# Kernel tuning notes

Hardware: AMD Instinct MI355X
Metric: run time of the kernel (lower is better)

## Reference

```python
import jax, jax.numpy as jnp
import numpy as np

N = 100000   # num nodes
E = 3200000  # num edges (avg degree 32)
EPS = 1e-5   # BatchNorm eps


def _gcn_norm(edge_index, edge_weight, n):
    # add self loops with weight 1 (PyG gcn_norm default fill_value=1.0)
    loops = jnp.arange(n, dtype=edge_index.dtype)
    ei = jnp.concatenate([edge_index, jnp.stack([loops, loops])], axis=1)
    ew = jnp.concatenate([edge_weight, jnp.ones((n,), edge_weight.dtype)])
    row, col = ei[0], ei[1]
    deg = jax.ops.segment_sum(ew, col, num_segments=n)
    deg_safe = jnp.where(deg > 0, deg, 1.0)
    dinv = jnp.where(deg > 0, jax.lax.rsqrt(deg_safe), 0.0)
    norm = dinv[row] * ew * dinv[col]  # [E+N]
    return row, col, norm


def _gcn_conv(x, row, col, norm, W, b, n):
    h = x @ W                                   # [N, out]
    msg = h[row] * norm[:, None]                # gather + scale, [E+N, out]
    out = jax.ops.segment_sum(msg, col, num_segments=n)  # scatter-add
    return out + b


def _bn(x, g, b, rm, rv):
    # BatchNorm1d in eval mode: running statistics
    return (x - rm) * jax.lax.rsqrt(rv + EPS) * g + b


def setup_inputs() -> dict:
    key = jax.random.key(0)
    ks = jax.random.split(key, 24)
    def p(i, shape, scale=1.0):
        return jax.random.normal(ks[i], shape, dtype=jnp.float32) * scale
    inp = {
        "x": p(0, (N, 1)),
        "edge_index": jax.random.randint(ks[1], (2, E), 0, N, dtype=jnp.int32),
        "edge_weight": jax.random.uniform(ks[2], (E,), dtype=jnp.float32),
        # GCNConv weights (glorot-ish scale) and biases
        "W1": p(3, (1, 16), 0.5), "b1": jnp.zeros((16,), jnp.float32),
        "W2": p(4, (16, 4), 0.25), "b2": jnp.zeros((4,), jnp.float32),
        "W3": p(5, (4, 1), 0.5), "b3": jnp.zeros((1,), jnp.float32),
        # BatchNorm params + running stats (running_var > 0)
        "g1": p(6, (16,), 0.1) + 1.0, "be1": p(7, (16,), 0.1),
        "rm1": p(8, (16,), 0.1), "rv1": jax.random.uniform(ks[9], (16,)) + 0.5,
        "g2": p(10, (4,), 0.1) + 1.0, "be2": p(11, (4,), 0.1),
        "rm2": p(12, (4,), 0.1), "rv2": jax.random.uniform(ks[13], (4,)) + 0.5,
        "g3": p(14, (1,), 0.1) + 1.0, "be3": p(15, (1,), 0.1),
        "rm3": p(16, (1,), 0.1), "rv3": jax.random.uniform(ks[17], (1,)) + 0.5,
        # end Linear(1, 1)
        "Wl": p(18, (1, 1)), "bl": p(19, (1,), 0.1),
    }
    return inp


def reference(x, edge_index, edge_weight,
              W1, b1, W2, b2, W3, b3,
              g1, be1, rm1, rv1,
              g2, be2, rm2, rv2,
              g3, be3, rm3, rv3,
              Wl, bl):
    row, col, norm = _gcn_norm(edge_index, edge_weight, N)
    h = _gcn_conv(x, row, col, norm, W1, b1, N)
    h = jax.nn.relu(_bn(h, g1, be1, rm1, rv1))  # dropout = identity in eval
    h = _gcn_conv(h, row, col, norm, W2, b2, N)
    h = jax.nn.relu(_bn(h, g2, be2, rm2, rv2))
    h = _gcn_conv(h, row, col, norm, W3, b3, N)
    h = _bn(h, g3, be3, rm3, rv3)
    h = h @ Wl + bl
    return jax.nn.sigmoid(h)
```

## Files before the change

kernel.cpp:

```cpp
#include <hip/hip_runtime.h>
#include <math.h>

#define NN 100000
#define NE 3200000
#define EPSBN 1e-5f

#define BSH 7
#define NB 782
#define NBLK 500
#define CHUNK 6400
#define C4 (CHUNK/4)
#define CAP 5120
#define BTA 512

#define STCAP 4608
#define NCOL 100096

__global__ void k_params_zero(const float* __restrict__ W1, const float* __restrict__ b1,
                              const float* __restrict__ g1, const float* __restrict__ be1,
                              const float* __restrict__ rm1, const float* __restrict__ rv1,
                              const float* __restrict__ b2,
                              const float* __restrict__ g2, const float* __restrict__ be2,
                              const float* __restrict__ rm2, const float* __restrict__ rv2,
                              const float* __restrict__ b3,
                              const float* __restrict__ g3, const float* __restrict__ be3,
                              const float* __restrict__ rm3, const float* __restrict__ rv3,
                              const float* __restrict__ Wl, const float* __restrict__ bl,
                              float* __restrict__ P, int* __restrict__ cnt) {
    int f = threadIdx.x;
    for (int i = f; i < NB; i += 1024) cnt[i] = 0;
    if (f < 16) {
        float k = g1[f] * rsqrtf(rv1[f] + EPSBN);
        P[f]      = W1[f] * k;
        P[16 + f] = (b1[f] - rm1[f]) * k + be1[f];
    }
    if (f < 4) {
        float k = g2[f] * rsqrtf(rv2[f] + EPSBN);
        P[32 + f] = k;
        P[36 + f] = (b2[f] - rm2[f]) * k + be2[f];
    }
    if (f == 0) {
        float k = g3[0] * rsqrtf(rv3[0] + EPSBN);
        P[40] = k * Wl[0];
        P[41] = ((b3[0] - rm3[0]) * k + be3[0]) * Wl[0] + bl[0];
    }
}

__global__ void k_build(const int* __restrict__ row, const int* __restrict__ col,
                        const float* __restrict__ ew, int* __restrict__ cnt,
                        uint2* __restrict__ rec) {
    __shared__ int h[NB];
    __shared__ int gb[NB];
    __shared__ int gsum[98];
    __shared__ uint2 st[CHUNK];
    __shared__ unsigned short sb[CHUNK];
    int blk = blockIdx.x, tid = threadIdx.x;
    for (int j = tid; j < NB; j += BTA) h[j] = 0;
    __syncthreads();

    const int4* c4 = (const int4*)(col + blk * CHUNK);
    int rk[4][4];
#pragma unroll
    for (int it = 0; it < 4; ++it) {
        int i = tid + it * BTA;
        if (i < C4) {
            int4 c = c4[i];
            rk[it][0] = atomicAdd(&h[c.x >> BSH], 1);
            rk[it][1] = atomicAdd(&h[c.y >> BSH], 1);
            rk[it][2] = atomicAdd(&h[c.z >> BSH], 1);
            rk[it][3] = atomicAdd(&h[c.w >> BSH], 1);
        }
    }
    __syncthreads();

    for (int j = tid; j < NB; j += BTA) {
        int hj = h[j];
        gb[j] = hj ? atomicAdd(&cnt[j], hj) : 0;
    }

    if (tid < 98) {
        int s = 0, b0 = tid * 8;
#pragma unroll
        for (int k = 0; k < 8; ++k) { int idx = b0 + k; s += (idx < NB) ? h[idx] : 0; }
        gsum[tid] = s;
    }
    __syncthreads();
    if (tid == 0) {
        int run = 0;
        for (int g = 0; g < 98; ++g) { int t = gsum[g]; gsum[g] = run; run += t; }
    }
    __syncthreads();
    if (tid < 98) {
        int run = gsum[tid], b0 = tid * 8;
#pragma unroll
        for (int k = 0; k < 8; ++k) {
            int idx = b0 + k;
            if (idx < NB) { int t = h[idx]; h[idx] = run; run += t; }
        }
    }
    __syncthreads();

    const int4*   r4 = (const int4*)(row + blk * CHUNK);
    const float4* w4 = (const float4*)(ew + blk * CHUNK);
#pragma unroll
    for (int it = 0; it < 4; ++it) {
        int i = tid + it * BTA;
        if (i < C4) {
            int4 c = c4[i]; int4 r = r4[i]; float4 w = w4[i];
            int b0 = c.x >> BSH, b1 = c.y >> BSH, b2 = c.z >> BSH, b3 = c.w >> BSH;
            int s0 = h[b0] + rk[it][0];
            st[s0] = make_uint2((unsigned)r.x | ((unsigned)(c.x & 127) << 17), __float_as_uint(w.x));
            sb[s0] = (unsigned short)b0;
            int s1 = h[b1] + rk[it][1];
            st[s1] = make_uint2((unsigned)r.y | ((unsigned)(c.y & 127) << 17), __float_as_uint(w.y));
            sb[s1] = (unsigned short)b1;
            int s2 = h[b2] + rk[it][2];
            st[s2] = make_uint2((unsigned)r.z | ((unsigned)(c.z & 127) << 17), __float_as_uint(w.z));
            sb[s2] = (unsigned short)b2;
            int s3 = h[b3] + rk[it][3];
            st[s3] = make_uint2((unsigned)r.w | ((unsigned)(c.w & 127) << 17), __float_as_uint(w.w));
            sb[s3] = (unsigned short)b3;
        }
    }
    __syncthreads();

    for (int i = tid; i < CHUNK; i += BTA) {
        int b = sb[i];
        rec[(size_t)b * CAP + gb[b] + (i - h[b])] = st[i];
    }
}

__global__ void k_subsort_deg(const int* __restrict__ cnt, uint2* __restrict__ rec,
                              int2* __restrict__ colsc, const float* __restrict__ x,
                              float* __restrict__ dinv, float* __restrict__ xd) {
    __shared__ uint2 st[STCAP];
    __shared__ int subtot[128];
    __shared__ int colbase[128];
    int bin = blockIdx.x, tid = threadIdx.x;
    int lane = tid & 63, wv = tid >> 6;
    int n = cnt[bin];
    if (n > STCAP) n = STCAP;
    uint2* rb = rec + (size_t)bin * CAP;

    uint2 r[9];
#pragma unroll
    for (int k = 0; k < 9; ++k) {
        int i = tid + k * BTA;
        if (i < n) r[k] = rb[i];
    }
    if (tid < 128) subtot[tid] = 0;
    __syncthreads();

    int rk[9];
#pragma unroll
    for (int k = 0; k < 9; ++k) {
        int i = tid + k * BTA;
        if (i < n) {
            unsigned key = (r[k].x >> 17) & 127u;
            rk[k] = atomicAdd(&subtot[key], 1);
        }
    }
    __syncthreads();

    if (wv == 0) {
        int a = subtot[2 * lane], b = subtot[2 * lane + 1];
        int s = a + b;
#pragma unroll
        for (int off = 1; off < 64; off <<= 1) {
            int t = __shfl_up(s, off);
            if (lane >= off) s += t;
        }
        int excl = s - (a + b);
        colbase[2 * lane] = excl;
        colbase[2 * lane + 1] = excl + a;
    }
    __syncthreads();

    if (tid < 128)
        colsc[bin * 128 + tid] = make_int2(bin * CAP + colbase[tid], subtot[tid]);

#pragma unroll
    for (int k = 0; k < 9; ++k) {
        int i = tid + k * BTA;
        if (i < n) {
            unsigned key = (r[k].x >> 17) & 127u;
            st[colbase[key] + rk[k]] = r[k];
        }
    }
    __syncthreads();

    for (int i = tid; i < n; i += BTA) rb[i] = st[i];

    for (int pass = 0; pass < 2; ++pass) {
        int cl = pass * 64 + (tid >> 3);
        int j = tid & 7;
        int cb = colbase[cl], cc = subtot[cl];
        float a = 0.f;
        for (int i = j; i < cc; i += 8) a += __uint_as_float(st[cb + i].y);
        a += __shfl_xor(a, 1); a += __shfl_xor(a, 2); a += __shfl_xor(a, 4);
        int colv = (bin << BSH) + cl;
        if (j == 0 && colv < NN) {
            float d = rsqrtf(1.0f + a);
            dinv[colv] = d;
            xd[colv] = x[colv] * d;
        }
    }
}


__global__ void k_agg1_8(const int2* __restrict__ colsc, const uint2* __restrict__ rec,
                         const float* __restrict__ dinv, const float* __restrict__ xd,
                         const float* __restrict__ P, const float* __restrict__ W2,
                         float* __restrict__ m2s) {
    int tid = threadIdx.x;
    int col = blockIdx.x * 64 + (tid >> 3);
    int j = tid & 7;
    if (col >= NN) return;
    int2 sc = colsc[col];
    const uint2* p = rec + sc.x;
    float a = 0.f;
    for (int i = j; i < sc.y; i += 8) {
        uint2 v = p[i];
        a += xd[v.x & 0x1FFFF] * __uint_as_float(v.y);
    }
    a += __shfl_xor(a, 1); a += __shfl_xor(a, 2); a += __shfl_xor(a, 4);
    if (j == 0) {
        float dc = dinv[col];
        float y = (a + xd[col]) * dc;
        float m0 = 0.f, m1 = 0.f, m2v = 0.f, m3v = 0.f;
#pragma unroll
        for (int f = 0; f < 16; ++f) {
            float z = fmaxf(fmaf(y, P[f], P[16 + f]), 0.0f);
            m0 = fmaf(z, W2[f * 4 + 0], m0);
            m1 = fmaf(z, W2[f * 4 + 1], m1);
            m2v = fmaf(z, W2[f * 4 + 2], m2v);
            m3v = fmaf(z, W2[f * 4 + 3], m3v);
        }
        *(float4*)(m2s + 4 * col) = make_float4(m0 * dc, m1 * dc, m2v * dc, m3v * dc);
    }
}

__global__ void k_agg2_8(const int2* __restrict__ colsc, const uint2* __restrict__ rec,
                         const float* __restrict__ dinv, const float* __restrict__ m2s,
                         const float* __restrict__ P, const float* __restrict__ W3,
                         float* __restrict__ m3s) {
    int tid = threadIdx.x;
    int col = blockIdx.x * 64 + (tid >> 3);
    int j = tid & 7;
    if (col >= NN) return;
    int2 sc = colsc[col];
    const uint2* p = rec + sc.x;
    float a0 = 0.f, a1 = 0.f, a2 = 0.f, a3 = 0.f;
    for (int i = j; i < sc.y; i += 8) {
        uint2 v = p[i];
        float w = __uint_as_float(v.y);
        float4 m = *(const float4*)(m2s + 4 * (v.x & 0x1FFFF));
        a0 = fmaf(m.x, w, a0);
        a1 = fmaf(m.y, w, a1);
        a2 = fmaf(m.z, w, a2);
        a3 = fmaf(m.w, w, a3);
    }
    a0 += __shfl_xor(a0, 1); a0 += __shfl_xor(a0, 2); a0 += __shfl_xor(a0, 4);
    a1 += __shfl_xor(a1, 1); a1 += __shfl_xor(a1, 2); a1 += __shfl_xor(a1, 4);
    a2 += __shfl_xor(a2, 1); a2 += __shfl_xor(a2, 2); a2 += __shfl_xor(a2, 4);
    a3 += __shfl_xor(a3, 1); a3 += __shfl_xor(a3, 2); a3 += __shfl_xor(a3, 4);
    if (j == 0) {
        float dc = dinv[col];
        float4 mc = *(const float4*)(m2s + 4 * col);
        float b0 = (a0 + mc.x) * dc;
        float b1 = (a1 + mc.y) * dc;
        float b2 = (a2 + mc.z) * dc;
        float b3 = (a3 + mc.w) * dc;
        float v3 = 0.f;
        v3 = fmaf(fmaxf(fmaf(b0, P[32], P[36]), 0.f), W3[0], v3);
        v3 = fmaf(fmaxf(fmaf(b1, P[33], P[37]), 0.f), W3[1], v3);
        v3 = fmaf(fmaxf(fmaf(b2, P[34], P[38]), 0.f), W3[2], v3);
        v3 = fmaf(fmaxf(fmaf(b3, P[35], P[39]), 0.f), W3[3], v3);
        m3s[col] = v3 * dc;
    }
}

__global__ void k_agg3_8(const int2* __restrict__ colsc, const uint2* __restrict__ rec,
                         const float* __restrict__ dinv, const float* __restrict__ m3s,
                         const float* __restrict__ P, float* __restrict__ out) {
    int tid = threadIdx.x;
    int col = blockIdx.x * 64 + (tid >> 3);
    int j = tid & 7;
    if (col >= NN) return;
    int2 sc = colsc[col];
    const uint2* p = rec + sc.x;
    float a = 0.f;
    for (int i = j; i < sc.y; i += 8) {
        uint2 v = p[i];
        a += m3s[v.x & 0x1FFFF] * __uint_as_float(v.y);
    }
    a += __shfl_xor(a, 1); a += __shfl_xor(a, 2); a += __shfl_xor(a, 4);
    if (j == 0) {
        float t = fmaf((a + m3s[col]) * dinv[col], P[40], P[41]);
        out[col] = 1.0f / (1.0f + __expf(-t));
    }
}


__global__ void k_init_deg(float* __restrict__ deg) {
    int i = blockIdx.x * blockDim.x + threadIdx.x;
    if (i < NN) deg[i] = 1.0f;
}

__global__ void k_dinv_y1(const float* __restrict__ deg, const float* __restrict__ x,
                          float* __restrict__ dinv, float* __restrict__ y1) {
    int i = blockIdx.x * blockDim.x + threadIdx.x;
    if (i >= NN) return;
    float d = rsqrtf(deg[i]);
    dinv[i] = d;
    y1[i] = x[i] * d * d;
}

__global__ void k_l1_epi(const float* __restrict__ y1, const float* __restrict__ dinv,
                         const float* __restrict__ P, const float* __restrict__ W2,
                         float* __restrict__ m2, float* __restrict__ agg2) {
    int i = blockIdx.x * blockDim.x + threadIdx.x;
    if (i >= NN) return;
    float y = y1[i];
    float m0 = 0.f, m1 = 0.f, m2v = 0.f, m3v = 0.f;
#pragma unroll
    for (int f = 0; f < 16; ++f) {
        float z = fmaxf(fmaf(y, P[f], P[16 + f]), 0.0f);
        m0 = fmaf(z, W2[f * 4 + 0], m0);
        m1 = fmaf(z, W2[f * 4 + 1], m1);
        m2v = fmaf(z, W2[f * 4 + 2], m2v);
        m3v = fmaf(z, W2[f * 4 + 3], m3v);
    }
    float d = dinv[i];
    float d2 = d * d;
    *(float4*)(m2 + 4 * i)   = make_float4(m0, m1, m2v, m3v);
    *(float4*)(agg2 + 4 * i) = make_float4(m0 * d2, m1 * d2, m2v * d2, m3v * d2);
}

__global__ void k_l2_epi(const float* __restrict__ agg2, const float* __restrict__ dinv,
                         const float* __restrict__ P, const float* __restrict__ W3,
                         float* __restrict__ m3, float* __restrict__ agg3) {
    int i = blockIdx.x * blockDim.x + threadIdx.x;
    if (i >= NN) return;
    float4 a = *(const float4*)(agg2 + 4 * i);
    float v = 0.f;
    v = fmaf(fmaxf(fmaf(a.x, P[32], P[36]), 0.f), W3[0], v);
    v = fmaf(fmaxf(fmaf(a.y, P[33], P[37]), 0.f), W3[1], v);
    v = fmaf(fmaxf(fmaf(a.z, P[34], P[38]), 0.f), W3[2], v);
    v = fmaf(fmaxf(fmaf(a.w, P[35], P[39]), 0.f), W3[3], v);
    float d = dinv[i];
    m3[i] = v;
    agg3[i] = v * d * d;
}

__global__ void k_final(const float* __restrict__ agg3, const float* __restrict__ P,
                        float* __restrict__ out) {
    int i = blockIdx.x * blockDim.x + threadIdx.x;
    if (i >= NN) return;
    float t = fmaf(agg3[i], P[40], P[41]);
    out[i] = 1.0f / (1.0f + __expf(-t));
}

__global__ void k_deg(const int* __restrict__ col, const float* __restrict__ ew,
                      float* __restrict__ deg) {
    int e = (blockIdx.x * blockDim.x + threadIdx.x) * 4;
    if (e >= NE) return;
    int4 c = *(const int4*)(col + e);
    float4 w = *(const float4*)(ew + e);
    atomicAdd(&deg[c.x], w.x);
    atomicAdd(&deg[c.y], w.y);
    atomicAdd(&deg[c.z], w.z);
    atomicAdd(&deg[c.w], w.w);
}

__global__ void k_norm_agg1(const int* __restrict__ row, const int* __restrict__ col,
                            const float* __restrict__ ew, const float* __restrict__ dinv,
                            const float* __restrict__ x,
                            float* __restrict__ norm, float* __restrict__ y1) {
    int e = (blockIdx.x * blockDim.x + threadIdx.x) * 4;
    if (e >= NE) return;
    int4 r = *(const int4*)(row + e);
    int4 c = *(const int4*)(col + e);
    float4 w = *(const float4*)(ew + e);
    float4 nv;
    nv.x = dinv[r.x] * w.x * dinv[c.x];
    nv.y = dinv[r.y] * w.y * dinv[c.y];
    nv.z = dinv[r.z] * w.z * dinv[c.z];
    nv.w = dinv[r.w] * w.w * dinv[c.w];
    *(float4*)(norm + e) = nv;
    atomicAdd(&y1[c.x], x[r.x] * nv.x);
    atomicAdd(&y1[c.y], x[r.y] * nv.y);
    atomicAdd(&y1[c.z], x[r.z] * nv.z);
    atomicAdd(&y1[c.w], x[r.w] * nv.w);
}

__global__ void k_agg2(const int* __restrict__ row, const int* __restrict__ col,
                       const float* __restrict__ norm, const float* __restrict__ m2,
                       float* __restrict__ agg2) {
    int e = blockIdx.x * blockDim.x + threadIdx.x;
    if (e >= NE) return;
    int r = row[e], c = col[e];
    float nv = norm[e];
    float4 m = *(const float4*)(m2 + 4 * r);
    atomicAdd(&agg2[4 * c + 0], m.x * nv);
    atomicAdd(&agg2[4 * c + 1], m.y * nv);
    atomicAdd(&agg2[4 * c + 2], m.z * nv);
    atomicAdd(&agg2[4 * c + 3], m.w * nv);
}

__global__ void k_agg3(const int* __restrict__ row, const int* __restrict__ col,
                       const float* __restrict__ norm, const float* __restrict__ m3,
                       float* __restrict__ agg3) {
    int e = (blockIdx.x * blockDim.x + threadIdx.x) * 4;
    if (e >= NE) return;
    int4 r = *(const int4*)(row + e);
    int4 c = *(const int4*)(col + e);
    float4 nv = *(const float4*)(norm + e);
    atomicAdd(&agg3[c.x], m3[r.x] * nv.x);
    atomicAdd(&agg3[c.y], m3[r.y] * nv.y);
    atomicAdd(&agg3[c.z], m3[r.z] * nv.z);
    atomicAdd(&agg3[c.w], m3[r.w] * nv.w);
}


extern "C" void kernel_launch(void* const* d_in, const int* in_sizes, int n_in,
                              void* d_out, int out_size, void* d_ws, size_t ws_size,
                              hipStream_t stream) {
    const float* x  = (const float*)d_in[0];
    const int*   ei = (const int*)d_in[1];
    const float* ew = (const float*)d_in[2];
    const float* W1 = (const float*)d_in[3];
    const float* b1 = (const float*)d_in[4];
    const float* W2 = (const float*)d_in[5];
    const float* b2 = (const float*)d_in[6];
    const float* W3 = (const float*)d_in[7];
    const float* b3 = (const float*)d_in[8];
    const float* g1 = (const float*)d_in[9];
    const float* be1 = (const float*)d_in[10];
    const float* rm1 = (const float*)d_in[11];
    const float* rv1 = (const float*)d_in[12];
    const float* g2 = (const float*)d_in[13];
    const float* be2 = (const float*)d_in[14];
    const float* rm2 = (const float*)d_in[15];
    const float* rv2 = (const float*)d_in[16];
    const float* g3 = (const float*)d_in[17];
    const float* be3 = (const float*)d_in[18];
    const float* rm3 = (const float*)d_in[19];
    const float* rv3 = (const float*)d_in[20];
    const float* Wl = (const float*)d_in[21];
    const float* bl = (const float*)d_in[22];
    float* out = (float*)d_out;

    const int* row = ei;
    const int* col = ei + NE;

    const int BT = 256;
    const int gN = (NN + BT - 1) / BT;
    const int gE4 = (NE / 4 + BT - 1) / BT;
    const int gC8 = NCOL / 64;

    char* ws = (char*)d_ws;

    if (ws_size >= 36800000u) {
        float* P     = (float*)(ws);
        int*   cnt   = (int*)  (ws + 4096);
        int2*  colsc = (int2*) (ws + 16384);
        float* dinv  = (float*)(ws + 1048576);
        float* xd    = (float*)(ws + 1572864);
        float* m3s   = (float*)(ws + 2097152);
        float* m2s   = (float*)(ws + 2621440);
        uint2* rec   = (uint2*)(ws + 4718592);

        k_params_zero<<<1, 1024, 0, stream>>>(W1, b1, g1, be1, rm1, rv1,
                                              b2, g2, be2, rm2, rv2,
                                              b3, g3, be3, rm3, rv3, Wl, bl, P, cnt);
        k_build<<<NBLK, BTA, 0, stream>>>(row, col, ew, cnt, rec);
        k_subsort_deg<<<NB, BTA, 0, stream>>>(cnt, rec, colsc, x, dinv, xd);
        k_agg1_8<<<gC8, BTA, 0, stream>>>(colsc, rec, dinv, xd, P, W2, m2s);
        k_agg2_8<<<gC8, BTA, 0, stream>>>(colsc, rec, dinv, m2s, P, W3, m3s);
        k_agg3_8<<<gC8, BTA, 0, stream>>>(colsc, rec, dinv, m3s, P, out);
    } else {
        float* deg   = (float*)(ws);
        float* dinv  = (float*)(ws + 400000);
        float* y1    = (float*)(ws + 800000);
        float* m2    = (float*)(ws + 1200000);
        float* agg2  = (float*)(ws + 2800000);
        float* m3    = (float*)(ws + 4400000);
        float* agg3  = (float*)(ws + 4800000);
        float* Pf    = (float*)(ws + 5200000);
        float* norm  = (float*)(ws + 5200256);
        const int gE1 = (NE + BT - 1) / BT;

        k_params_zero<<<1, 1024, 0, stream>>>(W1, b1, g1, be1, rm1, rv1,
                                              b2, g2, be2, rm2, rv2,
                                              b3, g3, be3, rm3, rv3, Wl, bl, Pf, (int*)(ws + 5300000));
        k_init_deg<<<gN, BT, 0, stream>>>(deg);
        k_deg<<<gE4, BT, 0, stream>>>(col, ew, deg);
        k_dinv_y1<<<gN, BT, 0, stream>>>(deg, x, dinv, y1);
        k_norm_agg1<<<gE4, BT, 0, stream>>>(row, col, ew, dinv, x, norm, y1);
        k_l1_epi<<<gN, BT, 0, stream>>>(y1, dinv, Pf, W2, m2, agg2);
        k_agg2<<<gE1, BT, 0, stream>>>(row, col, norm, m2, agg2);
        k_l2_epi<<<gN, BT, 0, stream>>>(agg2, dinv, Pf, W3, m3, agg3);
        k_agg3<<<gE4, BT, 0, stream>>>(row, col, norm, m3, agg3);
        k_final<<<gN, BT, 0, stream>>>(agg3, Pf, out);
    }
}
```

Baseline: 109.7 us.

## Vectorize record scatter/sort with 16-byte accesses and fold params kernel into subsort

The build kernel now packs the per-bin count and global base into one int2 and writes sorted records two at a time, reading 16 bytes of staging per thread. The subsort kernel loads and stores bin records as uint4 pairs instead of single uint2 values. The separate parameter kernel is removed: BN parameter folding moves into block 0 of the subsort kernel and the count reset becomes a memset, saving one launch. Writes in the build scatter remain 8-byte when adjacent records fall in different bins, and an odd record count needs a tail path.

```diff
diff --git a/kernel.cpp b/kernel.cpp
--- a/kernel.cpp
+++ b/kernel.cpp
@@ -49,13 +49,12 @@
 __global__ void k_build(const int* __restrict__ row, const int* __restrict__ col,
                         const float* __restrict__ ew, int* __restrict__ cnt,
                         uint2* __restrict__ rec) {
-    __shared__ int h[NB];
-    __shared__ int gb[NB];
+    __shared__ int2 hg[NB];
     __shared__ int gsum[98];
-    __shared__ uint2 st[CHUNK];
+    __shared__ __align__(16) uint2 st[CHUNK];
     __shared__ unsigned short sb[CHUNK];
     int blk = blockIdx.x, tid = threadIdx.x;
-    for (int j = tid; j < NB; j += BTA) h[j] = 0;
+    for (int j = tid; j < NB; j += BTA) hg[j].x = 0;
     __syncthreads();
 
     const int4* c4 = (const int4*)(col + blk * CHUNK);
@@ -65,23 +64,23 @@
         int i = tid + it * BTA;
         if (i < C4) {
             int4 c = c4[i];
-            rk[it][0] = atomicAdd(&h[c.x >> BSH], 1);
-            rk[it][1] = atomicAdd(&h[c.y >> BSH], 1);
-            rk[it][2] = atomicAdd(&h[c.z >> BSH], 1);
-            rk[it][3] = atomicAdd(&h[c.w >> BSH], 1);
+            rk[it][0] = atomicAdd(&hg[c.x >> BSH].x, 1);
+            rk[it][1] = atomicAdd(&hg[c.y >> BSH].x, 1);
+            rk[it][2] = atomicAdd(&hg[c.z >> BSH].x, 1);
+            rk[it][3] = atomicAdd(&hg[c.w >> BSH].x, 1);
         }
     }
     __syncthreads();
 
     for (int j = tid; j < NB; j += BTA) {
-        int hj = h[j];
-        gb[j] = hj ? atomicAdd(&cnt[j], hj) : 0;
+        int hj = hg[j].x;
+        hg[j].y = hj ? atomicAdd(&cnt[j], hj) : 0;
     }
 
     if (tid < 98) {
         int s = 0, b0 = tid * 8;
 #pragma unroll
-        for (int k = 0; k < 8; ++k) { int idx = b0 + k; s += (idx < NB) ? h[idx] : 0; }
+        for (int k = 0; k < 8; ++k) { int idx = b0 + k; s += (idx < NB) ? hg[idx].x : 0; }
         gsum[tid] = s;
     }
     __syncthreads();
@@ -95,7 +94,7 @@
 #pragma unroll
         for (int k = 0; k < 8; ++k) {
             int idx = b0 + k;
-            if (idx < NB) { int t = h[idx]; h[idx] = run; run += t; }
+            if (idx < NB) { int t = hg[idx].x; hg[idx].x = run; run += t; }
         }
     }
     __syncthreads();
@@ -108,32 +107,53 @@
         if (i < C4) {
             int4 c = c4[i]; int4 r = r4[i]; float4 w = w4[i];
             int b0 = c.x >> BSH, b1 = c.y >> BSH, b2 = c.z >> BSH, b3 = c.w >> BSH;
-            int s0 = h[b0] + rk[it][0];
+            int s0 = hg[b0].x + rk[it][0];
             st[s0] = make_uint2((unsigned)r.x | ((unsigned)(c.x & 127) << 17), __float_as_uint(w.x));
             sb[s0] = (unsigned short)b0;
-            int s1 = h[b1] + rk[it][1];
+            int s1 = hg[b1].x + rk[it][1];
             st[s1] = make_uint2((unsigned)r.y | ((unsigned)(c.y & 127) << 17), __float_as_uint(w.y));
             sb[s1] = (unsigned short)b1;
-            int s2 = h[b2] + rk[it][2];
+            int s2 = hg[b2].x + rk[it][2];
             st[s2] = make_uint2((unsigned)r.z | ((unsigned)(c.z & 127) << 17), __float_as_uint(w.z));
             sb[s2] = (unsigned short)b2;
-            int s3 = h[b3] + rk[it][3];
+            int s3 = hg[b3].x + rk[it][3];
             st[s3] = make_uint2((unsigned)r.w | ((unsigned)(c.w & 127) << 17), __float_as_uint(w.w));
             sb[s3] = (unsigned short)b3;
         }
     }
     __syncthreads();
 
-    for (int i = tid; i < CHUNK; i += BTA) {
-        int b = sb[i];
-        rec[(size_t)b * CAP + gb[b] + (i - h[b])] = st[i];
+    for (int p = tid; p < CHUNK / 2; p += BTA) {
+        uint4 two = ((const uint4*)st)[p];
+        unsigned tags = ((const unsigned*)sb)[p];
+        int b0 = (int)(tags & 0xFFFFu), b1 = (int)(tags >> 16);
+        int2 v0 = hg[b0];
+        int i0 = 2 * p - v0.x;
+        rec[(size_t)b0 * CAP + v0.y + i0] = make_uint2(two.x, two.y);
+        if (b1 == b0) {
+            rec[(size_t)b0 * CAP + v0.y + i0 + 1] = make_uint2(two.z, two.w);
+        } else {
+            int2 v1 = hg[b1];
+            rec[(size_t)b1 * CAP + v1.y + (2 * p + 1 - v1.x)] = make_uint2(two.z, two.w);
+        }
     }
 }
 
 __global__ void k_subsort_deg(const int* __restrict__ cnt, uint2* __restrict__ rec,
                               int2* __restrict__ colsc, const float* __restrict__ x,
-                              float* __restrict__ dinv, float* __restrict__ xd) {
-    __shared__ uint2 st[STCAP];
+                              float* __restrict__ dinv, float* __restrict__ xd,
+                              const float* __restrict__ W1, const float* __restrict__ b1,
+                              const float* __restrict__ g1, const float* __restrict__ be1,
+                              const float* __restrict__ rm1, const float* __restrict__ rv1,
+                              const float* __restrict__ b2,
+                              const float* __restrict__ g2, const float* __restrict__ be2,
+                              const float* __restrict__ rm2, const float* __restrict__ rv2,
+                              const float* __restrict__ b3,
+                              const float* __restrict__ g3, const float* __restrict__ be3,
+                              const float* __restrict__ rm3, const float* __restrict__ rv3,
+                              const float* __restrict__ Wl, const float* __restrict__ bl,
+                              float* __restrict__ P) {
+    __shared__ __align__(16) uint2 st[STCAP];
     __shared__ int subtot[128];
     __shared__ int colbase[128];
     int bin = blockIdx.x, tid = threadIdx.x;
@@ -142,23 +162,40 @@
     if (n > STCAP) n = STCAP;
     uint2* rb = rec + (size_t)bin * CAP;
 
-    uint2 r[9];
-#pragma unroll
-    for (int k = 0; k < 9; ++k) {
-        int i = tid + k * BTA;
-        if (i < n) r[k] = rb[i];
+    if (bin == 0) {
+        if (tid < 16) {
+            float k = g1[tid] * rsqrtf(rv1[tid] + EPSBN);
+            P[tid]      = W1[tid] * k;
+            P[16 + tid] = (b1[tid] - rm1[tid]) * k + be1[tid];
+        }
+        if (tid < 4) {
+            float k = g2[tid] * rsqrtf(rv2[tid] + EPSBN);
+            P[32 + tid] = k;
+            P[36 + tid] = (b2[tid] - rm2[tid]) * k + be2[tid];
+        }
+        if (tid == 0) {
+            float k = g3[0] * rsqrtf(rv3[0] + EPSBN);
+            P[40] = k * Wl[0];
+            P[41] = ((b3[0] - rm3[0]) * k + be3[0]) * Wl[0] + bl[0];
+        }
+    }
+
+    int np = (n + 1) >> 1;
+    uint4 r4[5];
+#pragma unroll
+    for (int k = 0; k < 5; ++k) {
+        int p = tid + k * BTA;
+        if (p < np) r4[k] = ((const uint4*)rb)[p];
     }
     if (tid < 128) subtot[tid] = 0;
     __syncthreads();
 
-    int rk[9];
-#pragma unroll
-    for (int k = 0; k < 9; ++k) {
-        int i = tid + k * BTA;
-        if (i < n) {
-            unsigned key = (r[k].x >> 17) & 127u;
-            rk[k] = atomicAdd(&subtot[key], 1);
-        }
+    int rk0[5], rk1[5];
+#pragma unroll
+    for (int k = 0; k < 5; ++k) {
+        int i0 = 2 * (tid + k * BTA);
+        if (i0 < n)     rk0[k] = atomicAdd(&subtot[(r4[k].x >> 17) & 127u], 1);
+        if (i0 + 1 < n) rk1[k] = atomicAdd(&subtot[(r4[k].z >> 17) & 127u], 1);
     }
     __syncthreads();
 
@@ -180,16 +217,22 @@
         colsc[bin * 128 + tid] = make_int2(bin * CAP + colbase[tid], subtot[tid]);
 
 #pragma unroll
-    for (int k = 0; k < 9; ++k) {
-        int i = tid + k * BTA;
-        if (i < n) {
-            unsigned key = (r[k].x >> 17) & 127u;
-            st[colbase[key] + rk[k]] = r[k];
-        }
-    }
-    __syncthreads();
-
-    for (int i = tid; i < n; i += BTA) rb[i] = st[i];
+    for (int k = 0; k < 5; ++k) {
+        int i0 = 2 * (tid + k * BTA);
+        if (i0 < n) {
+            unsigned key = (r4[k].x >> 17) & 127u;
+            st[colbase[key] + rk0[k]] = make_uint2(r4[k].x, r4[k].y);
+        }
+        if (i0 + 1 < n) {
+            unsigned key = (r4[k].z >> 17) & 127u;
+            st[colbase[key] + rk1[k]] = make_uint2(r4[k].z, r4[k].w);
+        }
+    }
+    __syncthreads();
+
+    for (int p = tid; p < (n >> 1); p += BTA)
+        ((uint4*)rb)[p] = ((const uint4*)st)[p];
+    if ((n & 1) && tid == 0) rb[n - 1] = st[n - 1];
 
     for (int pass = 0; pass < 2; ++pass) {
         int cl = pass * 64 + (tid >> 3);
@@ -471,11 +514,12 @@
         float* m2s   = (float*)(ws + 2621440);
         uint2* rec   = (uint2*)(ws + 4718592);
 
-        k_params_zero<<<1, 1024, 0, stream>>>(W1, b1, g1, be1, rm1, rv1,
+        hipMemsetAsync(cnt, 0, NB * sizeof(int), stream);
+        k_build<<<NBLK, BTA, 0, stream>>>(row, col, ew, cnt, rec);
+        k_subsort_deg<<<NB, BTA, 0, stream>>>(cnt, rec, colsc, x, dinv, xd,
+                                              W1, b1, g1, be1, rm1, rv1,
                                               b2, g2, be2, rm2, rv2,
-                                              b3, g3, be3, rm3, rv3, Wl, bl, P, cnt);
-        k_build<<<NBLK, BTA, 0, stream>>>(row, col, ew, cnt, rec);
-        k_subsort_deg<<<NB, BTA, 0, stream>>>(cnt, rec, colsc, x, dinv, xd);
+                                              b3, g3, be3, rm3, rv3, Wl, bl, P);
         k_agg1_8<<<gC8, BTA, 0, stream>>>(colsc, rec, dinv, xd, P, W2, m2s);
         k_agg2_8<<<gC8, BTA, 0, stream>>>(colsc, rec, dinv, m2s, P, W3, m3s);
         k_agg3_8<<<gC8, BTA, 0, stream>>>(colsc, rec, dinv, m3s, P, out);
```

Result: slower. 113.5 us (+3.4%).

## Replace global-atomic bucketing with per-block local sort and offset-table gather

Applied to the files above, without the earlier changes.

The build kernel now sorts each edge chunk by destination bin entirely in shared memory and writes the chunk contiguously, plus a per-block bin offset table, instead of using global atomics on bin counters to scatter records. The subsort kernel then gathers each bin's segments from all 500 chunks using that table, sorts by column, and writes to a second record buffer. Parameter folding is moved into the subsort kernel, which removes the separate zeroing and params launch. This trades global atomic contention and scattered writes for a larger workspace and many short, fragmented reads in the gather stage. The new path only runs when the workspace is at least about 65.6 MB.

```diff
diff --git a/kernel.cpp b/kernel.cpp
--- a/kernel.cpp
+++ b/kernel.cpp
@@ -46,6 +46,231 @@
     }
 }
 
+
+__global__ void k_build2(const int* __restrict__ row, const int* __restrict__ col,
+                         const float* __restrict__ ew, int* __restrict__ bh,
+                         uint2* __restrict__ rec) {
+    __shared__ int h[NB];
+    __shared__ int gsum[98];
+    __shared__ __align__(16) uint2 st[CHUNK];
+    int blk = blockIdx.x, tid = threadIdx.x;
+    for (int j = tid; j < NB; j += BTA) h[j] = 0;
+    __syncthreads();
+
+    const int4* c4 = (const int4*)(col + blk * CHUNK);
+    int rk[4][4];
+#pragma unroll
+    for (int it = 0; it < 4; ++it) {
+        int i = tid + it * BTA;
+        if (i < C4) {
+            int4 c = c4[i];
+            rk[it][0] = atomicAdd(&h[c.x >> BSH], 1);
+            rk[it][1] = atomicAdd(&h[c.y >> BSH], 1);
+            rk[it][2] = atomicAdd(&h[c.z >> BSH], 1);
+            rk[it][3] = atomicAdd(&h[c.w >> BSH], 1);
+        }
+    }
+    __syncthreads();
+
+    if (tid < 98) {
+        int s = 0, b0 = tid * 8;
+#pragma unroll
+        for (int k = 0; k < 8; ++k) { int idx = b0 + k; s += (idx < NB) ? h[idx] : 0; }
+        gsum[tid] = s;
+    }
+    __syncthreads();
+    if (tid == 0) {
+        int run = 0;
+        for (int g = 0; g < 98; ++g) { int t = gsum[g]; gsum[g] = run; run += t; }
+    }
+    __syncthreads();
+    if (tid < 98) {
+        int run = gsum[tid], b0 = tid * 8;
+#pragma unroll
+        for (int k = 0; k < 8; ++k) {
+            int idx = b0 + k;
+            if (idx < NB) { int t = h[idx]; h[idx] = run; run += t; }
+        }
+    }
+    __syncthreads();
+
+    for (int j = tid; j < NB; j += BTA) bh[blk * NB + j] = h[j];
+
+    const int4*   r4 = (const int4*)(row + blk * CHUNK);
+    const float4* w4 = (const float4*)(ew + blk * CHUNK);
+#pragma unroll
+    for (int it = 0; it < 4; ++it) {
+        int i = tid + it * BTA;
+        if (i < C4) {
+            int4 c = c4[i]; int4 r = r4[i]; float4 w = w4[i];
+            int b0 = c.x >> BSH, b1 = c.y >> BSH, b2 = c.z >> BSH, b3 = c.w >> BSH;
+            st[h[b0] + rk[it][0]] =
+                make_uint2((unsigned)r.x | ((unsigned)(c.x & 127) << 17), __float_as_uint(w.x));
+            st[h[b1] + rk[it][1]] =
+                make_uint2((unsigned)r.y | ((unsigned)(c.y & 127) << 17), __float_as_uint(w.y));
+            st[h[b2] + rk[it][2]] =
+                make_uint2((unsigned)r.z | ((unsigned)(c.z & 127) << 17), __float_as_uint(w.z));
+            st[h[b3] + rk[it][3]] =
+                make_uint2((unsigned)r.w | ((unsigned)(c.w & 127) << 17), __float_as_uint(w.w));
+        }
+    }
+    __syncthreads();
+
+    uint4* dst = (uint4*)(rec + (size_t)blk * CHUNK);
+    const uint4* src = (const uint4*)st;
+    for (int p = tid; p < CHUNK / 2; p += BTA) dst[p] = src[p];
+}
+
+__global__ void k_subsort2(const int* __restrict__ bh, const uint2* __restrict__ rec,
+                           uint2* __restrict__ rec2, int2* __restrict__ colsc,
+                           const float* __restrict__ x,
+                           float* __restrict__ dinv, float* __restrict__ xd,
+                           const float* __restrict__ W1, const float* __restrict__ b1,
+                           const float* __restrict__ g1, const float* __restrict__ be1,
+                           const float* __restrict__ rm1, const float* __restrict__ rv1,
+                           const float* __restrict__ b2,
+                           const float* __restrict__ g2, const float* __restrict__ be2,
+                           const float* __restrict__ rm2, const float* __restrict__ rv2,
+                           const float* __restrict__ b3,
+                           const float* __restrict__ g3, const float* __restrict__ be3,
+                           const float* __restrict__ rm3, const float* __restrict__ rv3,
+                           const float* __restrict__ Wl, const float* __restrict__ bl,
+                           float* __restrict__ P) {
+    __shared__ __align__(16) uint2 st[STCAP];
+    __shared__ int loff[NBLK];
+    __shared__ int scnt[NBLK];
+    __shared__ int soff[NBLK];
+    __shared__ int subtot[128];
+    __shared__ int colbase[128];
+    __shared__ int ntot_s;
+    int bin = blockIdx.x, tid = threadIdx.x;
+    int lane = tid & 63, wv = tid >> 6;
+
+    if (bin == 0) {
+        if (tid < 16) {
+            float k = g1[tid] * rsqrtf(rv1[tid] + EPSBN);
+            P[tid]      = W1[tid] * k;
+            P[16 + tid] = (b1[tid] - rm1[tid]) * k + be1[tid];
+        }
+        if (tid < 4) {
+            float k = g2[tid] * rsqrtf(rv2[tid] + EPSBN);
+            P[32 + tid] = k;
+            P[36 + tid] = (b2[tid] - rm2[tid]) * k + be2[tid];
+        }
+        if (tid == 0) {
+            float k = g3[0] * rsqrtf(rv3[0] + EPSBN);
+            P[40] = k * Wl[0];
+            P[41] = ((b3[0] - rm3[0]) * k + be3[0]) * Wl[0] + bl[0];
+        }
+    }
+
+    for (int s = tid; s < NBLK; s += BTA) {
+        int a = bh[s * NB + bin];
+        int b = (bin + 1 < NB) ? bh[s * NB + bin + 1] : CHUNK;
+        loff[s] = a;
+        scnt[s] = b - a;
+    }
+    __syncthreads();
+
+    if (wv == 0) {
+        int b8 = lane * 8;
+        int c[8]; int t = 0;
+#pragma unroll
+        for (int k = 0; k < 8; ++k) {
+            int idx = b8 + k;
+            c[k] = (idx < NBLK) ? scnt[idx] : 0;
+            t += c[k];
+        }
+        int s = t;
+#pragma unroll
+        for (int off = 1; off < 64; off <<= 1) {
+            int u = __shfl_up(s, off);
+            if (lane >= off) s += u;
+        }
+        int run = s - t;
+#pragma unroll
+        for (int k = 0; k < 8; ++k) {
+            int idx = b8 + k;
+            if (idx < NBLK) { soff[idx] = run; run += c[k]; }
+        }
+        if (lane == 63) ntot_s = s;
+    }
+    __syncthreads();
+    int n = ntot_s;
+    if (n > STCAP) n = STCAP;
+
+    {
+        int grp = tid >> 3, j8 = tid & 7;
+        for (int s = grp; s < NBLK; s += 64) {
+            int len = scnt[s];
+            const uint2* src = rec + (size_t)s * CHUNK + loff[s];
+            int dst = soff[s];
+            for (int i = j8; i < len; i += 8) st[dst + i] = src[i];
+        }
+    }
+    __syncthreads();
+
+    uint2 r[9];
+#pragma unroll
+    for (int k = 0; k < 9; ++k) {
+        int i = tid + k * BTA;
+        if (i < n) r[k] = st[i];
+    }
+    if (tid < 128) subtot[tid] = 0;
+    __syncthreads();
+
+    int rk[9];
+#pragma unroll
+    for (int k = 0; k < 9; ++k) {
+        int i = tid + k * BTA;
+        if (i < n) rk[k] = atomicAdd(&subtot[(r[k].x >> 17) & 127u], 1);
+    }
+    __syncthreads();
+
+    if (wv == 0) {
+        int a = subtot[2 * lane], b = subtot[2 * lane + 1];
+        int s = a + b;
+#pragma unroll
+        for (int off = 1; off < 64; off <<= 1) {
+            int t = __shfl_up(s, off);
+            if (lane >= off) s += t;
+        }
+        int excl = s - (a + b);
+        colbase[2 * lane] = excl;
+        colbase[2 * lane + 1] = excl + a;
+    }
+    __syncthreads();
+
+    if (tid < 128)
+        colsc[bin * 128 + tid] = make_int2(bin * CAP + colbase[tid], subtot[tid]);
+
+#pragma unroll
+    for (int k = 0; k < 9; ++k) {
+        int i = tid + k * BTA;
+        if (i < n) st[colbase[(r[k].x >> 17) & 127u] + rk[k]] = r[k];
+    }
+    __syncthreads();
+
+    uint2* rb = rec2 + (size_t)bin * CAP;
+    for (int i = tid; i < n; i += BTA) rb[i] = st[i];
+
+    for (int pass = 0; pass < 2; ++pass) {
+        int cl = pass * 64 + (tid >> 3);
+        int j = tid & 7;
+        int cb = colbase[cl], cc = subtot[cl];
+        float a = 0.f;
+        for (int i = j; i < cc; i += 8) a += __uint_as_float(st[cb + i].y);
+        a += __shfl_xor(a, 1); a += __shfl_xor(a, 2); a += __shfl_xor(a, 4);
+        int colv = (bin << BSH) + cl;
+        if (j == 0 && colv < NN) {
+            float d = rsqrtf(1.0f + a);
+            dinv[colv] = d;
+            xd[colv] = x[colv] * d;
+        }
+    }
+}
+
+
 __global__ void k_build(const int* __restrict__ row, const int* __restrict__ col,
                         const float* __restrict__ ew, int* __restrict__ cnt,
                         uint2* __restrict__ rec) {
@@ -155,10 +380,7 @@
 #pragma unroll
     for (int k = 0; k < 9; ++k) {
         int i = tid + k * BTA;
-        if (i < n) {
-            unsigned key = (r[k].x >> 17) & 127u;
-            rk[k] = atomicAdd(&subtot[key], 1);
-        }
+        if (i < n) rk[k] = atomicAdd(&subtot[(r[k].x >> 17) & 127u], 1);
     }
     __syncthreads();
 
@@ -182,10 +404,7 @@
 #pragma unroll
     for (int k = 0; k < 9; ++k) {
         int i = tid + k * BTA;
-        if (i < n) {
-            unsigned key = (r[k].x >> 17) & 127u;
-            st[colbase[key] + rk[k]] = r[k];
-        }
+        if (i < n) st[colbase[(r[k].x >> 17) & 127u] + rk[k]] = r[k];
     }
     __syncthreads();
 
@@ -461,7 +680,26 @@
 
     char* ws = (char*)d_ws;
 
-    if (ws_size >= 36800000u) {
+    if (ws_size >= 65600000u) {
+        float* P     = (float*)(ws);
+        int2*  colsc = (int2*) (ws + 16384);
+        float* dinv  = (float*)(ws + 1048576);
+        float* xd    = (float*)(ws + 1572864);
+        float* m3s   = (float*)(ws + 2097152);
+        float* m2s   = (float*)(ws + 2621440);
+        int*   bh    = (int*)  (ws + 4221952);
+        uint2* rec   = (uint2*)(ws + 6291456);
+        uint2* rec2  = (uint2*)(ws + 33554432);
+
+        k_build2<<<NBLK, BTA, 0, stream>>>(row, col, ew, bh, rec);
+        k_subsort2<<<NB, BTA, 0, stream>>>(bh, rec, rec2, colsc, x, dinv, xd,
+                                           W1, b1, g1, be1, rm1, rv1,
+                                           b2, g2, be2, rm2, rv2,
+                                           b3, g3, be3, rm3, rv3, Wl, bl, P);
+        k_agg1_8<<<gC8, BTA, 0, stream>>>(colsc, rec2, dinv, xd, P, W2, m2s);
+        k_agg2_8<<<gC8, BTA, 0, stream>>>(colsc, rec2, dinv, m2s, P, W3, m3s);
+        k_agg3_8<<<gC8, BTA, 0, stream>>>(colsc, rec2, dinv, m3s, P, out);
+    } else if (ws_size >= 36800000u) {
         float* P     = (float*)(ws);
         int*   cnt   = (int*)  (ws + 4096);
         int2*  colsc = (int2*) (ws + 16384);
```

Result: slower. 112.2 us (+2.3%).
